# Optimization experiments

Measured on AMD Instinct MI355X. Metric: run time of the kernel, lower is better.

## Reference

```python
import jax, jax.numpy as jnp
import numpy as np

B, L, S, H, C = 64, 512, 512, 768, 9  # batch, bert subword len, word seq len, hidden, num_classes


def setup_inputs() -> dict:
    key = jax.random.key(0)
    k1, k2, k3 = jax.random.split(key, 3)
    rng = np.random.RandomState(0)
    # per-word subword counts in {1,2,3}; truncate so totals fit in L subword slots
    lens = rng.randint(1, 4, size=(B, S))
    cum = lens.cumsum(axis=1)
    keep = cum <= L
    ids_lens = (lens * keep).astype(np.int32)
    totals = ids_lens.sum(axis=1)
    attention_mask = (np.arange(L)[None, :] < totals[:, None]).astype(np.int32)
    label_mask = ids_lens > 0
    label_ids = (rng.randint(0, C, size=(B, S)) * label_mask).astype(np.int32)
    bert_out = jax.random.normal(k1, (B, L, H), dtype=jnp.float32)
    W = jax.random.normal(k2, (H, C), dtype=jnp.float32) * 0.02
    b = jnp.zeros((C,), dtype=jnp.float32)
    return {
        "bert_out": bert_out,
        "W": W,
        "b": b,
        "attention_mask": jnp.asarray(attention_mask),
        "ids_lens": jnp.asarray(ids_lens),
        "label_ids": jnp.asarray(label_ids),
        "label_mask": jnp.asarray(label_mask),
    }


def reference(bert_out, W, b, attention_mask, ids_lens, label_ids, label_mask):
    Bv, Lv, Hv = bert_out.shape
    Sv = ids_lens.shape[1]
    nseg = Bv * Sv
    am = attention_mask.astype(jnp.int32)
    # subword position within each example's valid region
    sidx = jnp.cumsum(am, axis=1) - 1                       # [B, L]
    # word index for each subword: searchsorted into cumulative word lengths
    ends = jnp.cumsum(ids_lens, axis=1)                     # [B, S]
    widx = jax.vmap(lambda e, s: jnp.searchsorted(e, s, side='right'))(ends, sidx)
    seg = jnp.where(am > 0, widx + jnp.arange(Bv)[:, None] * Sv, nseg)  # pad bucket = nseg
    flat = bert_out.reshape(Bv * Lv, Hv)
    segf = seg.reshape(Bv * Lv)
    sums = jax.ops.segment_sum(flat, segf, num_segments=nseg + 1)[:nseg]
    cnts = jax.ops.segment_sum(jnp.ones((Bv * Lv,), bert_out.dtype), segf,
                               num_segments=nseg + 1)[:nseg]
    mean = sums / jnp.maximum(cnts, 1.0)[:, None]           # segment mean (split().mean(0))
    word_mask = (ids_lens > 0).reshape(nseg)
    embed = jnp.where(word_mask[:, None], mean, 0.0).reshape(Bv, Sv, Hv)  # masked_scatter
    # dropout in eval mode = identity
    logits = embed @ W + b                                  # [B, S, C]
    logp = jax.nn.log_softmax(logits, axis=-1)
    lab = jnp.clip(label_ids, 0, W.shape[1] - 1)
    nll = -jnp.take_along_axis(logp, lab[..., None].astype(jnp.int32), axis=-1)[..., 0]
    valid = label_mask.astype(bert_out.dtype)
    loss = jnp.sum(nll * valid) / jnp.maximum(jnp.sum(valid), 1.0)
    pred = jnp.argmax(logits, axis=-1)
    return loss, pred
```

## Files before the change

kernel.cpp:

```cpp
#include <hip/hip_runtime.h>

#define BB 64
#define LL 512
#define SS 512
#define HH 768
#define CC 9
#define NWORDS (BB * SS)
#define NWAVES 8
#define WPW 8
#define WORDS_PER_BLOCK (NWAVES * WPW)
#define WBLOCKS (NWORDS / WORDS_PER_BLOCK)
#define WTPAD 772
#define LGPAD 13

__global__ __launch_bounds__(512) void scan_kernel(const int* __restrict__ ids_lens,
                                                   int* __restrict__ starts,
                                                   float* __restrict__ accum) {
    __shared__ int buf[SS];
    int b = blockIdx.x, t = threadIdx.x;
    int v = ids_lens[b * SS + t];
    buf[t] = v;
    __syncthreads();
    for (int off = 1; off < SS; off <<= 1) {
        int x = (t >= off) ? buf[t - off] : 0;
        __syncthreads();
        buf[t] += x;
        __syncthreads();
    }
    starts[b * SS + t] = buf[t] - v;
    if (b == 0 && t == 0) { accum[0] = 0.0f; ((int*)accum)[1] = 0; }
}

__device__ __forceinline__ void acc3(const float* __restrict__ p, float m[12]) {
#pragma unroll
    for (int c3 = 0; c3 < 3; c3++) {
        float4 u = *reinterpret_cast<const float4*>(p + c3 * 256);
        m[c3 * 4 + 0] += u.x;
        m[c3 * 4 + 1] += u.y;
        m[c3 * 4 + 2] += u.z;
        m[c3 * 4 + 3] += u.w;
    }
}

template <int CTRL>
__device__ __forceinline__ float dpp_add(float x) {
    int y = __builtin_amdgcn_update_dpp(0, __float_as_int(x), CTRL, 0xf, 0xf, true);
    return x + __int_as_float(y);
}
__device__ __forceinline__ float rsum64(float x) {
    x = dpp_add<0x111>(x);
    x = dpp_add<0x112>(x);
    x = dpp_add<0x114>(x);
    x = dpp_add<0x118>(x);
    x = dpp_add<0x142>(x);
    x = dpp_add<0x143>(x);
    return x;
}

__global__ __launch_bounds__(512) void word_kernel(
    const float* __restrict__ bert,
    const float* __restrict__ Wm,
    const float* __restrict__ bias,
    const int* __restrict__ ids_lens,
    const int* __restrict__ label_ids,
    const int* __restrict__ starts,
    float* __restrict__ pred_out,
    float* __restrict__ accum)
{
    __shared__ __align__(16) float WT[CC][WTPAD];
    __shared__ float LG[WORDS_PER_BLOCK][LGPAD];

    for (int i = threadIdx.x; i < HH * CC; i += 512) {
        int h = i / CC;
        int c = i - h * CC;
        WT[c][h] = Wm[i];
    }
    __syncthreads();

    int wave = threadIdx.x >> 6;
    int lane = threadIdx.x & 63;
    int hoff = lane * 4;
    int gblock = blockIdx.x * WORDS_PER_BLOCK;
    int bidx = gblock >> 9;
    int gbase = gblock + wave * WPW;

#pragma unroll
    for (int p = 0; p < WPW / 2; ++p) {
        int ga = gbase + 2 * p;
        int gb = ga + 1;
        int lena = ids_lens[ga], lenb = ids_lens[gb];
        int sta = starts[ga], stb = starts[gb];

        float ma[12], mb[12];
#pragma unroll
        for (int i = 0; i < 12; i++) { ma[i] = 0.0f; mb[i] = 0.0f; }

        const float* pa = bert + ((size_t)bidx * LL + sta) * HH + hoff;
        const float* pb = bert + ((size_t)bidx * LL + stb) * HH + hoff;
        if (lena > 0) acc3(pa, ma);
        if (lena > 1) acc3(pa + HH, ma);
        if (lena > 2) acc3(pa + 2 * HH, ma);
        if (lenb > 0) acc3(pb, mb);
        if (lenb > 1) acc3(pb + HH, mb);
        if (lenb > 2) acc3(pb + 2 * HH, mb);

        float inva = 1.0f / (float)(lena > 0 ? lena : 1);
        float invb = 1.0f / (float)(lenb > 0 ? lenb : 1);
#pragma unroll
        for (int i = 0; i < 12; i++) { ma[i] *= inva; mb[i] *= invb; }

        float la[CC], lb[CC];
#pragma unroll
        for (int c = 0; c < CC; c++) { la[c] = 0.0f; lb[c] = 0.0f; }
#pragma unroll
        for (int c3 = 0; c3 < 3; c3++) {
#pragma unroll
            for (int c = 0; c < CC; c++) {
                float4 wv = *reinterpret_cast<const float4*>(&WT[c][c3 * 256 + hoff]);
                la[c] += ma[c3 * 4 + 0] * wv.x + ma[c3 * 4 + 1] * wv.y
                       + ma[c3 * 4 + 2] * wv.z + ma[c3 * 4 + 3] * wv.w;
                lb[c] += mb[c3 * 4 + 0] * wv.x + mb[c3 * 4 + 1] * wv.y
                       + mb[c3 * 4 + 2] * wv.z + mb[c3 * 4 + 3] * wv.w;
            }
        }

#pragma unroll
        for (int c = 0; c < CC; c++) { la[c] = rsum64(la[c]); lb[c] = rsum64(lb[c]); }
        int wa = wave * WPW + 2 * p;
        if (lane == 63) {
#pragma unroll
            for (int c = 0; c < CC; c++) {
                LG[wa][c] = la[c];
                LG[wa + 1][c] = lb[c];
            }
        }
    }

    __syncthreads();

    if (threadIdx.x < WORDS_PER_BLOCK) {
        int w = threadIdx.x;
        int g = gblock + w;
        float lg[CC];
#pragma unroll
        for (int c = 0; c < CC; c++) lg[c] = LG[w][c] + bias[c];

        float mx = lg[0];
        int arg = 0;
#pragma unroll
        for (int c = 1; c < CC; c++) {
            if (lg[c] > mx) { mx = lg[c]; arg = c; }
        }
        float se = 0.0f;
#pragma unroll
        for (int c = 0; c < CC; c++) se += expf(lg[c] - mx);
        float lse = mx + logf(se);

        int len = ids_lens[g];
        int lab = label_ids[g];
        lab = lab < 0 ? 0 : (lab > CC - 1 ? CC - 1 : lab);
        int valid = (len > 0) ? 1 : 0;
        float nll = (lse - lg[lab]) * (float)valid;

        pred_out[g] = (float)arg;

        float s = nll;
        int cn = valid;
#pragma unroll
        for (int off = 32; off > 0; off >>= 1) {
            s += __shfl_xor(s, off, 64);
            cn += __shfl_xor(cn, off, 64);
        }
        if (w == 0) {
            atomicAdd(accum, s);
            atomicAdd((int*)accum + 1, cn);
        }
    }
}

__global__ void finalize_kernel(const float* __restrict__ accum,
                                float* __restrict__ out_loss) {
    float s = accum[0];
    int c = ((const int*)accum)[1];
    out_loss[0] = s / fmaxf((float)c, 1.0f);
}

extern "C" void kernel_launch(void* const* d_in, const int* in_sizes, int n_in,
                              void* d_out, int out_size, void* d_ws, size_t ws_size,
                              hipStream_t stream) {
    const float* bert = (const float*)d_in[0];
    const float* Wm   = (const float*)d_in[1];
    const float* bias = (const float*)d_in[2];
    const int* ids_lens  = (const int*)d_in[4];
    const int* label_ids = (const int*)d_in[5];

    float* out = (float*)d_out;

    int*   starts = (int*)d_ws;
    float* accum  = (float*)((char*)d_ws + NWORDS * sizeof(int));

    scan_kernel<<<BB, SS, 0, stream>>>(ids_lens, starts, accum);
    word_kernel<<<WBLOCKS, 512, 0, stream>>>(bert, Wm, bias, ids_lens, label_ids,
                                             starts, out + 1, accum);
    finalize_kernel<<<1, 1, 0, stream>>>(accum, out);
}
```

Before: 172.6 us.

## Project every subword row to logits first, then pool logits per word

Because mean pooling and the linear projection are both linear, the order is swapped. Every bert row is now projected to 9 logits in a dense streaming kernel, which reads all rows including padding. A second per-example kernel fuses the prefix scan, the segment mean over the small logit rows, the softmax/NLL and a last-block finalize. This removes the scan and finalize launches and the data-dependent gathers, at the cost of projecting padded rows and writing and reading a small intermediate buffer.

Result: no change. 170.5 us (-1.2%).

```diff
diff --git a/kernel.cpp b/kernel.cpp
--- a/kernel.cpp
+++ b/kernel.cpp
@@ -5,42 +5,12 @@
 #define SS 512
 #define HH 768
 #define CC 9
+#define NROWS (BB * LL)
 #define NWORDS (BB * SS)
-#define NWAVES 8
-#define WPW 8
-#define WORDS_PER_BLOCK (NWAVES * WPW)
-#define WBLOCKS (NWORDS / WORDS_PER_BLOCK)
+#define RLS 12
 #define WTPAD 772
-#define LGPAD 13
-
-__global__ __launch_bounds__(512) void scan_kernel(const int* __restrict__ ids_lens,
-                                                   int* __restrict__ starts,
-                                                   float* __restrict__ accum) {
-    __shared__ int buf[SS];
-    int b = blockIdx.x, t = threadIdx.x;
-    int v = ids_lens[b * SS + t];
-    buf[t] = v;
-    __syncthreads();
-    for (int off = 1; off < SS; off <<= 1) {
-        int x = (t >= off) ? buf[t - off] : 0;
-        __syncthreads();
-        buf[t] += x;
-        __syncthreads();
-    }
-    starts[b * SS + t] = buf[t] - v;
-    if (b == 0 && t == 0) { accum[0] = 0.0f; ((int*)accum)[1] = 0; }
-}
-
-__device__ __forceinline__ void acc3(const float* __restrict__ p, float m[12]) {
-#pragma unroll
-    for (int c3 = 0; c3 < 3; c3++) {
-        float4 u = *reinterpret_cast<const float4*>(p + c3 * 256);
-        m[c3 * 4 + 0] += u.x;
-        m[c3 * 4 + 1] += u.y;
-        m[c3 * 4 + 2] += u.z;
-        m[c3 * 4 + 3] += u.w;
-    }
-}
+#define R1_BLOCKS 1024
+#define ROWS_PER_BLOCK 32
 
 template <int CTRL>
 __device__ __forceinline__ float dpp_add(float x) {
@@ -57,20 +27,15 @@
     return x;
 }
 
-__global__ __launch_bounds__(512) void word_kernel(
+__global__ __launch_bounds__(256) void row_gemm_kernel(
     const float* __restrict__ bert,
     const float* __restrict__ Wm,
-    const float* __restrict__ bias,
-    const int* __restrict__ ids_lens,
-    const int* __restrict__ label_ids,
-    const int* __restrict__ starts,
-    float* __restrict__ pred_out,
+    float* __restrict__ RL,
     float* __restrict__ accum)
 {
     __shared__ __align__(16) float WT[CC][WTPAD];
-    __shared__ float LG[WORDS_PER_BLOCK][LGPAD];
 
-    for (int i = threadIdx.x; i < HH * CC; i += 512) {
+    for (int i = threadIdx.x; i < HH * CC; i += 256) {
         int h = i / CC;
         int c = i - h * CC;
         WT[c][h] = Wm[i];
@@ -80,109 +45,136 @@
     int wave = threadIdx.x >> 6;
     int lane = threadIdx.x & 63;
     int hoff = lane * 4;
-    int gblock = blockIdx.x * WORDS_PER_BLOCK;
-    int bidx = gblock >> 9;
-    int gbase = gblock + wave * WPW;
+
+    float4 wreg[CC][3];
+#pragma unroll
+    for (int c = 0; c < CC; c++)
+#pragma unroll
+        for (int c3 = 0; c3 < 3; c3++)
+            wreg[c][c3] = *reinterpret_cast<const float4*>(&WT[c][c3 * 256 + hoff]);
+
+    size_t row0 = (size_t)blockIdx.x * ROWS_PER_BLOCK + wave * 8;
 
 #pragma unroll
-    for (int p = 0; p < WPW / 2; ++p) {
-        int ga = gbase + 2 * p;
-        int gb = ga + 1;
-        int lena = ids_lens[ga], lenb = ids_lens[gb];
-        int sta = starts[ga], stb = starts[gb];
+    for (int r = 0; r < 8; ++r) {
+        const float* p = bert + (row0 + r) * HH + hoff;
+        float4 f0 = *reinterpret_cast<const float4*>(p);
+        float4 f1 = *reinterpret_cast<const float4*>(p + 256);
+        float4 f2 = *reinterpret_cast<const float4*>(p + 512);
 
-        float ma[12], mb[12];
+        float acc[CC];
 #pragma unroll
-        for (int i = 0; i < 12; i++) { ma[i] = 0.0f; mb[i] = 0.0f; }
+        for (int c = 0; c < CC; c++) {
+            acc[c] = f0.x * wreg[c][0].x + f0.y * wreg[c][0].y
+                   + f0.z * wreg[c][0].z + f0.w * wreg[c][0].w
+                   + f1.x * wreg[c][1].x + f1.y * wreg[c][1].y
+                   + f1.z * wreg[c][1].z + f1.w * wreg[c][1].w
+                   + f2.x * wreg[c][2].x + f2.y * wreg[c][2].y
+                   + f2.z * wreg[c][2].z + f2.w * wreg[c][2].w;
+        }
+#pragma unroll
+        for (int c = 0; c < CC; c++) acc[c] = rsum64(acc[c]);
 
-        const float* pa = bert + ((size_t)bidx * LL + sta) * HH + hoff;
-        const float* pb = bert + ((size_t)bidx * LL + stb) * HH + hoff;
-        if (lena > 0) acc3(pa, ma);
-        if (lena > 1) acc3(pa + HH, ma);
-        if (lena > 2) acc3(pa + 2 * HH, ma);
-        if (lenb > 0) acc3(pb, mb);
-        if (lenb > 1) acc3(pb + HH, mb);
-        if (lenb > 2) acc3(pb + 2 * HH, mb);
-
-        float inva = 1.0f / (float)(lena > 0 ? lena : 1);
-        float invb = 1.0f / (float)(lenb > 0 ? lenb : 1);
-#pragma unroll
-        for (int i = 0; i < 12; i++) { ma[i] *= inva; mb[i] *= invb; }
-
-        float la[CC], lb[CC];
-#pragma unroll
-        for (int c = 0; c < CC; c++) { la[c] = 0.0f; lb[c] = 0.0f; }
-#pragma unroll
-        for (int c3 = 0; c3 < 3; c3++) {
-#pragma unroll
-            for (int c = 0; c < CC; c++) {
-                float4 wv = *reinterpret_cast<const float4*>(&WT[c][c3 * 256 + hoff]);
-                la[c] += ma[c3 * 4 + 0] * wv.x + ma[c3 * 4 + 1] * wv.y
-                       + ma[c3 * 4 + 2] * wv.z + ma[c3 * 4 + 3] * wv.w;
-                lb[c] += mb[c3 * 4 + 0] * wv.x + mb[c3 * 4 + 1] * wv.y
-                       + mb[c3 * 4 + 2] * wv.z + mb[c3 * 4 + 3] * wv.w;
-            }
-        }
-
-#pragma unroll
-        for (int c = 0; c < CC; c++) { la[c] = rsum64(la[c]); lb[c] = rsum64(lb[c]); }
-        int wa = wave * WPW + 2 * p;
         if (lane == 63) {
-#pragma unroll
-            for (int c = 0; c < CC; c++) {
-                LG[wa][c] = la[c];
-                LG[wa + 1][c] = lb[c];
-            }
+            float* dst = RL + (row0 + r) * RLS;
+            float4 s0; s0.x = acc[0]; s0.y = acc[1]; s0.z = acc[2]; s0.w = acc[3];
+            float4 s1; s1.x = acc[4]; s1.y = acc[5]; s1.z = acc[6]; s1.w = acc[7];
+            *reinterpret_cast<float4*>(dst) = s0;
+            *reinterpret_cast<float4*>(dst + 4) = s1;
+            dst[8] = acc[8];
         }
     }
 
-    __syncthreads();
-
-    if (threadIdx.x < WORDS_PER_BLOCK) {
-        int w = threadIdx.x;
-        int g = gblock + w;
-        float lg[CC];
-#pragma unroll
-        for (int c = 0; c < CC; c++) lg[c] = LG[w][c] + bias[c];
-
-        float mx = lg[0];
-        int arg = 0;
-#pragma unroll
-        for (int c = 1; c < CC; c++) {
-            if (lg[c] > mx) { mx = lg[c]; arg = c; }
-        }
-        float se = 0.0f;
-#pragma unroll
-        for (int c = 0; c < CC; c++) se += expf(lg[c] - mx);
-        float lse = mx + logf(se);
-
-        int len = ids_lens[g];
-        int lab = label_ids[g];
-        lab = lab < 0 ? 0 : (lab > CC - 1 ? CC - 1 : lab);
-        int valid = (len > 0) ? 1 : 0;
-        float nll = (lse - lg[lab]) * (float)valid;
-
-        pred_out[g] = (float)arg;
-
-        float s = nll;
-        int cn = valid;
-#pragma unroll
-        for (int off = 32; off > 0; off >>= 1) {
-            s += __shfl_xor(s, off, 64);
-            cn += __shfl_xor(cn, off, 64);
-        }
-        if (w == 0) {
-            atomicAdd(accum, s);
-            atomicAdd((int*)accum + 1, cn);
-        }
+    if (blockIdx.x == 0 && threadIdx.x == 0) {
+        accum[0] = 0.0f;
+        accum[1] = 0.0f;
+        ((int*)accum)[2] = 0;
     }
 }
 
-__global__ void finalize_kernel(const float* __restrict__ accum,
-                                float* __restrict__ out_loss) {
-    float s = accum[0];
-    int c = ((const int*)accum)[1];
-    out_loss[0] = s / fmaxf((float)c, 1.0f);
+__global__ __launch_bounds__(512) void pool_kernel(
+    const float* __restrict__ RL,
+    const float* __restrict__ bias,
+    const int* __restrict__ ids_lens,
+    const int* __restrict__ label_ids,
+    float* __restrict__ pred_out,
+    float* __restrict__ accum,
+    float* __restrict__ out_loss)
+{
+    __shared__ int sbuf[SS];
+    __shared__ float swn[8], swc[8];
+
+    int b = blockIdx.x, t = threadIdx.x;
+    int lane = t & 63, wave = t >> 6;
+
+    int v = ids_lens[b * SS + t];
+    sbuf[t] = v;
+    __syncthreads();
+    for (int off = 1; off < SS; off <<= 1) {
+        int x = (t >= off) ? sbuf[t - off] : 0;
+        __syncthreads();
+        sbuf[t] += x;
+        __syncthreads();
+    }
+    int len = v;
+    int start = sbuf[t] - v;
+
+    float s[CC];
+#pragma unroll
+    for (int c = 0; c < CC; c++) s[c] = 0.0f;
+
+    const float* rl = RL + ((size_t)b * LL + start) * RLS;
+    for (int j = 0; j < len; ++j) {
+        const float* p = rl + j * RLS;
+        float4 a = *reinterpret_cast<const float4*>(p);
+        float4 c4 = *reinterpret_cast<const float4*>(p + 4);
+        float e = p[8];
+        s[0] += a.x;  s[1] += a.y;  s[2] += a.z;  s[3] += a.w;
+        s[4] += c4.x; s[5] += c4.y; s[6] += c4.z; s[7] += c4.w;
+        s[8] += e;
+    }
+
+    float inv = 1.0f / (float)(len > 0 ? len : 1);
+    float lg[CC];
+#pragma unroll
+    for (int c = 0; c < CC; c++) lg[c] = s[c] * inv + bias[c];
+
+    float mx = lg[0];
+    int arg = 0;
+#pragma unroll
+    for (int c = 1; c < CC; c++) {
+        if (lg[c] > mx) { mx = lg[c]; arg = c; }
+    }
+    float se = 0.0f;
+#pragma unroll
+    for (int c = 0; c < CC; c++) se += expf(lg[c] - mx);
+    float lse = mx + logf(se);
+
+    int lab = label_ids[b * SS + t];
+    lab = lab < 0 ? 0 : (lab > CC - 1 ? CC - 1 : lab);
+    float valid = (len > 0) ? 1.0f : 0.0f;
+    float nll = (lse - lg[lab]) * valid;
+
+    pred_out[b * SS + t] = (float)arg;
+
+    float rn = rsum64(nll);
+    float rc = rsum64(valid);
+    if (lane == 63) { swn[wave] = rn; swc[wave] = rc; }
+    __syncthreads();
+    if (t == 0) {
+        float bn = 0.0f, bc = 0.0f;
+#pragma unroll
+        for (int i = 0; i < 8; i++) { bn += swn[i]; bc += swc[i]; }
+        atomicAdd(accum, bn);
+        atomicAdd(accum + 1, bc);
+        __threadfence();
+        int old = atomicAdd((int*)accum + 2, 1);
+        if (old == BB - 1) {
+            float tn = atomicAdd(accum, 0.0f);
+            float tc = atomicAdd(accum + 1, 0.0f);
+            out_loss[0] = tn / fmaxf(tc, 1.0f);
+        }
+    }
 }
 
 extern "C" void kernel_launch(void* const* d_in, const int* in_sizes, int n_in,
@@ -196,11 +188,10 @@
 
     float* out = (float*)d_out;
 
-    int*   starts = (int*)d_ws;
-    float* accum  = (float*)((char*)d_ws + NWORDS * sizeof(int));
+    float* RL    = (float*)d_ws;
+    float* accum = RL + (size_t)NROWS * RLS;
 
-    scan_kernel<<<BB, SS, 0, stream>>>(ids_lens, starts, accum);
-    word_kernel<<<WBLOCKS, 512, 0, stream>>>(bert, Wm, bias, ids_lens, label_ids,
-                                             starts, out + 1, accum);
-    finalize_kernel<<<1, 1, 0, stream>>>(accum, out);
+    row_gemm_kernel<<<R1_BLOCKS, 256, 0, stream>>>(bert, Wm, RL, accum);
+    pool_kernel<<<BB, SS, 0, stream>>>(RL, bias, ids_lens, label_ids,
+                                       out + 1, accum, out);
 }
```
